# Kernel tuning notes

Measured on AMD Instinct MI355X. Metric: run time of the kernel, lower is better.

Reference implementation:

```python
import jax, jax.numpy as jnp
import numpy as np

B, Q, L = 256, 32, 40      # batch, num concept queries, text seq len
VW, TW, D = 768, 768, 256  # vision width, text width, contrastive embed dim


def setup_inputs() -> dict:
    key = jax.random.key(0)
    ks = jax.random.split(key, 5)
    concept_feat = jax.random.normal(ks[0], (B, Q, VW), jnp.float32)
    text_embeds = jax.random.normal(ks[1], (B, L, TW), jnp.float32)
    # contiguous attention masks: [CLS] tok ... [SEP] pad pad
    lengths = jax.random.randint(ks[2], (B,), 8, L + 1)
    text_mask = (jnp.arange(L)[None, :] < lengths[:, None]).astype(jnp.int32)
    Wc = jax.random.normal(ks[3], (VW, D), jnp.float32) * 0.02
    bc = jnp.zeros((D,), jnp.float32)
    Ww = jax.random.normal(ks[4], (TW, D), jnp.float32) * 0.02
    bw = jnp.zeros((D,), jnp.float32)
    temp_cpt = jnp.float32(0.07)
    return {"concept_feat": concept_feat, "text_embeds": text_embeds,
            "text_mask": text_mask, "Wc": Wc, "bc": bc, "Ww": Ww, "bw": bw,
            "temp_cpt": temp_cpt}


def _l2norm(x):
    return x / jnp.linalg.norm(x, axis=-1, keepdims=True)


def _remove_cls_sep(mask):
    # zero [CLS] (pos 0) and [SEP] (last nonzero position)
    m = mask.at[:, 0].set(0)
    Ls = m.shape[1]
    sep = (Ls - 1) - jnp.argmax(m[:, ::-1] > 0, axis=1)  # max nonzero index
    return m * (1 - jax.nn.one_hot(sep, Ls, dtype=m.dtype))


def _pair_sim(ref, ref_mask, cand, cand_mask):
    # ref: [Br,Sr,D] plays the 'visual_output' role, cand: [Bc,Sc,D] the
    # 'sequence_output' role of max_region_sum_word, vectorized over Br.
    A = jnp.einsum('bsd,ctd->bcst', ref, cand)  # [Br,Bc,Sr,Sc]
    valid = (ref_mask[:, None, :, None] > 0) & (cand_mask[None, :, None, :] > 0)
    A = jnp.where(valid, A, jnp.asarray(-2.0, A.dtype))
    row = A.max(axis=2)                          # [Br,Bc,Sc] max over ref pos
    n_words = (row > -2).sum(-1).astype(A.dtype)
    row = jnp.where(row < -1, 0.0, row).sum(-1) / n_words
    col = A.max(axis=3)                          # [Br,Bc,Sr] max over cand pos
    n_ref = (col > -2).sum(-1).astype(A.dtype)
    col = jnp.where(col < -1, 0.0, col).sum(-1) / n_ref
    return row + col                             # [Br,Bc]


def reference(concept_feat, text_embeds, text_mask, Wc, bc, Ww, bw, temp_cpt):
    cf = _l2norm(concept_feat @ Wc + bc)   # [B,Q,D]
    wf = _l2norm(text_embeds @ Ww + bw)    # [B,L,D]
    c_mask = jnp.ones(cf.shape[:-1], jnp.int32)
    w_mask = _remove_cls_sep(text_mask)
    # single device: AllGather is identity, rank 0
    sim_i2t = _pair_sim(cf, c_mask, wf, w_mask) / temp_cpt  # [B,B]
    sim_t2i = _pair_sim(wf, w_mask, cf, c_mask) / temp_cpt  # [B,B]
    # diagonal one-hot targets -> loss is -mean(diag(log_softmax))
    loss_i2t = -jnp.mean(jnp.diagonal(jax.nn.log_softmax(sim_i2t, axis=1)))
    loss_t2i = -jnp.mean(jnp.diagonal(jax.nn.log_softmax(sim_t2i, axis=1)))
    return (loss_i2t + loss_t2i) / 2
```

## Files before the change

kernel.cpp:

```cpp
#include <hip/hip_runtime.h>
#include <hip/hip_bf16.h>
#include <stdint.h>


using f32x4  = __attribute__((ext_vector_type(4))) float;
using bf16x8 = __attribute__((ext_vector_type(8))) short;
typedef unsigned uint32x2 __attribute__((ext_vector_type(2)));

__device__ __forceinline__ short f2bf(float f) {
  union { float f; uint32_t u; } x; x.f = f;
  uint32_t r = x.u + 0x7FFFu + ((x.u >> 16) & 1u);
  return (short)(r >> 16);
}

__device__ __forceinline__ bf16x8 pack8pk(float4 v0, float4 v1) {
  union { uint32_t u[4]; bf16x8 v; } r;
  asm("v_cvt_pk_bf16_f32 %0, %1, %2" : "=v"(r.u[0]) : "v"(v0.x), "v"(v0.y));
  asm("v_cvt_pk_bf16_f32 %0, %1, %2" : "=v"(r.u[1]) : "v"(v0.z), "v"(v0.w));
  asm("v_cvt_pk_bf16_f32 %0, %1, %2" : "=v"(r.u[2]) : "v"(v1.x), "v"(v1.y));
  asm("v_cvt_pk_bf16_f32 %0, %1, %2" : "=v"(r.u[3]) : "v"(v1.z), "v"(v1.w));
  return r.v;
}

__device__ __forceinline__ void gl_lds16(const unsigned short* g, unsigned short* l) {
  __builtin_amdgcn_global_load_lds(
      (const __attribute__((address_space(1))) void*)g,
      (__attribute__((address_space(3))) void*)l, 16, 0, 0);
}

template <int CTRL>
__device__ __forceinline__ float dppf(float x) {
  return __int_as_float(__builtin_amdgcn_update_dpp(
      0, __float_as_int(x), CTRL, 0xF, 0xF, true));
}
__device__ __forceinline__ float max16(float x) {
  x = fmaxf(x, dppf<0xB1>(x));
  x = fmaxf(x, dppf<0x4E>(x));
  x = fmaxf(x, dppf<0x141>(x));
  x = fmaxf(x, dppf<0x140>(x));
  return x;
}
__device__ __forceinline__ float sum16(float x) {
  x += dppf<0xB1>(x);
  x += dppf<0x4E>(x);
  x += dppf<0x141>(x);
  x += dppf<0x140>(x);
  return x;
}
__device__ __forceinline__ float rowsum_to63(float x) {
  x += dppf<0x142>(x);
  x += dppf<0x143>(x);
  return x;
}

#if __has_builtin(__builtin_amdgcn_permlane16_swap)
__device__ __forceinline__ float plmax16(float x) {
  uint32x2 r = __builtin_amdgcn_permlane16_swap(__float_as_uint(x), __float_as_uint(x), false, false);
  return fmaxf(__uint_as_float(r[0]), __uint_as_float(r[1]));
}
#else
__device__ __forceinline__ float plmax16(float x) { return fmaxf(x, __shfl_xor(x, 16)); }
#endif
#if __has_builtin(__builtin_amdgcn_permlane32_swap)
__device__ __forceinline__ float plmax32(float x) {
  uint32x2 r = __builtin_amdgcn_permlane32_swap(__float_as_uint(x), __float_as_uint(x), false, false);
  return fmaxf(__uint_as_float(r[0]), __uint_as_float(r[1]));
}
#else
__device__ __forceinline__ float plmax32(float x) { return fmaxf(x, __shfl_xor(x, 32)); }
#endif

__global__ __launch_bounds__(256) void k_trw(const float* __restrict__ Wc,
                                             const float* __restrict__ Ww,
                                             const int* __restrict__ tm,
                                             unsigned short* __restrict__ Wct,
                                             unsigned short* __restrict__ Wwt,
                                             unsigned long long* __restrict__ mb,
                                             float* __restrict__ nw) {
  __shared__ float tile[32][33];
  if (blockIdx.x == 0) {
    int b = threadIdx.x;
    unsigned long long bits = 0ull;
    int sep = -1;
    #pragma unroll
    for (int t = 1; t < 40; ++t) {
      if (tm[b * 40 + t] > 0) { bits |= (1ull << t); sep = t; }
    }
    if (sep >= 0) bits &= ~(1ull << sep);
    mb[b] = bits;
    nw[b] = 1.0f / (float)__popcll(bits);
  }
  int blk = blockIdx.x;
  const float* W; unsigned short* O;
  if (blk < 192) { W = Wc; O = Wct; } else { W = Ww; O = Wwt; blk -= 192; }
  const int tk = blk >> 3, td = blk & 7;
  const int k0 = tk * 32, d0 = td * 32;
  const int t = threadIdx.x;
  const int r = t >> 3, cq = (t & 7) * 4;
  float4 v = *(const float4*)(W + (size_t)(k0 + r) * 256 + d0 + cq);
  tile[r][cq] = v.x; tile[r][cq + 1] = v.y; tile[r][cq + 2] = v.z; tile[r][cq + 3] = v.w;
  __syncthreads();
  ushort4 o;
  o.x = (unsigned short)f2bf(tile[cq + 0][r]);
  o.y = (unsigned short)f2bf(tile[cq + 1][r]);
  o.z = (unsigned short)f2bf(tile[cq + 2][r]);
  o.w = (unsigned short)f2bf(tile[cq + 3][r]);
  *(ushort4*)(O + (size_t)(d0 + r) * 768 + k0 + cq) = o;
}

__global__ __launch_bounds__(256) void k_proj(const float* __restrict__ Xc,
                                              const float* __restrict__ Xt,
                                              const unsigned short* __restrict__ Wct,
                                              const unsigned short* __restrict__ Wwt,
                                              const float* __restrict__ bc,
                                              const float* __restrict__ bw,
                                              unsigned short* __restrict__ CFb,
                                              unsigned short* __restrict__ WFb) {
  __shared__ unsigned short As[32 * 768];
  __shared__ float red[32][4];
  const int blk = blockIdx.x;
  const float* X; const unsigned short* Wtb; const float* bias;
  unsigned short* out; int m0;
  if (blk < 256) { X = Xc; Wtb = Wct; bias = bc; out = CFb; m0 = blk * 32; }
  else           { X = Xt; Wtb = Wwt; bias = bw; out = WFb; m0 = (blk - 256) * 32; }

  const int t = threadIdx.x;
  #pragma unroll
  for (int i = 0; i < 12; ++i) {
    int ch = i * 256 + t;
    int r = ch / 96, c = ch - r * 96;
    const float* p = X + (size_t)(m0 + r) * 768 + c * 8;
    bf16x8 v = pack8pk(*(const float4*)p, *(const float4*)(p + 4));
    *(bf16x8*)(&As[r * 768 + ((c ^ (r & 7)) * 8)]) = v;
  }
  __syncthreads();

  const int w = t >> 6, l = t & 63;
  const int lr = l & 15, lg = l >> 4;
  const int n0 = w * 64;

  f32x4 acc[2][4];
  #pragma unroll
  for (int mi = 0; mi < 2; ++mi)
    #pragma unroll
    for (int ni = 0; ni < 4; ++ni) acc[mi][ni] = f32x4{0.f, 0.f, 0.f, 0.f};

  const int r0 = lr, r1 = 16 + lr;

  #pragma unroll 4
  for (int ks = 0; ks < 24; ++ks) {
    const int c16 = ks * 4 + lg;
    bf16x8 a0 = *(const bf16x8*)(&As[r0 * 768 + ((c16 ^ (r0 & 7)) * 8)]);
    bf16x8 a1 = *(const bf16x8*)(&As[r1 * 768 + ((c16 ^ (r1 & 7)) * 8)]);
    bf16x8 bb[4];
    #pragma unroll
    for (int ni = 0; ni < 4; ++ni)
      bb[ni] = *(const bf16x8*)(Wtb + (size_t)(n0 + ni * 16 + lr) * 768 + ks * 32 + lg * 8);
    #pragma unroll
    for (int ni = 0; ni < 4; ++ni)
      acc[0][ni] = __builtin_amdgcn_mfma_f32_16x16x32_bf16(a0, bb[ni], acc[0][ni], 0, 0, 0);
    #pragma unroll
    for (int ni = 0; ni < 4; ++ni)
      acc[1][ni] = __builtin_amdgcn_mfma_f32_16x16x32_bf16(a1, bb[ni], acc[1][ni], 0, 0, 0);
  }

  float bv[4];
  #pragma unroll
  for (int ni = 0; ni < 4; ++ni) bv[ni] = bias[n0 + ni * 16 + lr];

  float ss[2][4];
  #pragma unroll
  for (int mi = 0; mi < 2; ++mi)
    #pragma unroll
    for (int j = 0; j < 4; ++j) {
      float s = 0.f;
      #pragma unroll
      for (int ni = 0; ni < 4; ++ni) {
        acc[mi][ni][j] += bv[ni];
        s += acc[mi][ni][j] * acc[mi][ni][j];
      }
      ss[mi][j] = s;
    }
  #pragma unroll
  for (int m = 1; m <= 8; m <<= 1)
    #pragma unroll
    for (int mi = 0; mi < 2; ++mi)
      #pragma unroll
      for (int j = 0; j < 4; ++j)
        ss[mi][j] += __shfl_xor(ss[mi][j], m);
  if (lr == 0) {
    #pragma unroll
    for (int mi = 0; mi < 2; ++mi)
      #pragma unroll
      for (int j = 0; j < 4; ++j)
        red[mi * 16 + lg * 4 + j][w] = ss[mi][j];
  }
  __syncthreads();
  #pragma unroll
  for (int mi = 0; mi < 2; ++mi)
    #pragma unroll
    for (int j = 0; j < 4; ++j) {
      int r = mi * 16 + lg * 4 + j;
      float sc = rsqrtf(red[r][0] + red[r][1] + red[r][2] + red[r][3]);
      #pragma unroll
      for (int ni = 0; ni < 4; ++ni)
        out[(size_t)(m0 + r) * 256 + n0 + ni * 16 + lr] =
            (unsigned short)f2bf(acc[mi][ni][j] * sc);
    }
}

__global__ __launch_bounds__(512, 2) void k_pair(const unsigned short* __restrict__ CF,
                                                 const unsigned short* __restrict__ WF,
                                                 const unsigned long long* __restrict__ MB,
                                                 const float* __restrict__ NW,
                                                 const float* __restrict__ TEMP,
                                                 float* __restrict__ S,
                                                 float* __restrict__ St) {
  __shared__ unsigned short wfs[40960];
  const int tid = threadIdx.x;
  const int w = tid >> 6, l = tid & 63;
  const int lr = l & 15, lg = l >> 4;
  const int b0 = blockIdx.x * 16, c0 = blockIdx.y * 16;
  const float invt = 1.0f / TEMP[0];
  const float s32 = invt * 0.03125f;

  const int sti = w >> 1, sth = w & 1;
  {
    const int cq = c0;
    #pragma unroll
    for (int j = 0; j < 10; ++j) {
      int t = sth * 20 + j * 2 + (l >> 5), sl = l & 31;
      gl_lds16(WF + ((size_t)(cq + sti) * 40 + t) * 256 + ((sl ^ (t & 7)) * 8),
               &wfs[sti * 10240 + sth * 5120 + j * 512]);
    }
  }

  bf16x8 a[2][2][8];
  #pragma unroll
  for (int bi = 0; bi < 2; ++bi) {
    const int b = b0 + w * 2 + bi;
    #pragma unroll
    for (int mi = 0; mi < 2; ++mi)
      #pragma unroll
      for (int ks = 0; ks < 8; ++ks)
        a[bi][mi][ks] = *(const bf16x8*)(CF + (size_t)(b * 32 + mi * 16 + lr) * 256 + (ks * 4 + lg) * 8);
  }

  int lbase[3][2];
  #pragma unroll
  for (int ni = 0; ni < 3; ++ni) {
    int t = ni * 16 + lr; if (t > 39) t = 39;
    int x = t & 7;
    #pragma unroll
    for (int p = 0; p < 2; ++p)
      lbase[ni][p] = t * 512 + ((lg ^ (x & 3)) * 16) + ((p ^ ((x >> 2) & 1)) * 64);
  }
  const char* ldsb = (const char*)wfs;

  asm volatile("s_waitcnt vmcnt(0)" ::: "memory");
  __syncthreads();

  #pragma unroll 1
  for (int pn = 0; pn < 4; ++pn) {
    const int cq = c0 + pn * 4;
    if (pn > 0) {
      __syncthreads();
      #pragma unroll
      for (int j = 0; j < 10; ++j) {
        int t = sth * 20 + j * 2 + (l >> 5), sl = l & 31;
        gl_lds16(WF + ((size_t)(cq + sti) * 40 + t) * 256 + ((sl ^ (t & 7)) * 8),
                 &wfs[sti * 10240 + sth * 5120 + j * 512]);
      }
      asm volatile("s_waitcnt vmcnt(0)" ::: "memory");
      __syncthreads();
    }

    #pragma unroll
    for (int ci = 0; ci < 4; ++ci) {
      const int cg = cq + ci;

      f32x4 acc[2][2][3];
      #pragma unroll
      for (int bi = 0; bi < 2; ++bi)
        #pragma unroll
        for (int mi = 0; mi < 2; ++mi)
          #pragma unroll
          for (int ni = 0; ni < 3; ++ni) acc[bi][mi][ni] = f32x4{0.f, 0.f, 0.f, 0.f};

      __builtin_amdgcn_s_setprio(1);
      #pragma unroll
      for (int ks = 0; ks < 8; ++ks) {
        const int p = ks & 1, k = ks >> 1;
        bf16x8 bfv[3];
        #pragma unroll
        for (int ni = 0; ni < 3; ++ni)
          bfv[ni] = *(const bf16x8*)(ldsb + lbase[ni][p] + k * 128 + ci * 20480);
        #pragma unroll
        for (int bi = 0; bi < 2; ++bi)
          #pragma unroll
          for (int mi = 0; mi < 2; ++mi)
            #pragma unroll
            for (int ni = 0; ni < 3; ++ni)
              acc[bi][mi][ni] = __builtin_amdgcn_mfma_f32_16x16x32_bf16(a[bi][mi][ks], bfv[ni], acc[bi][mi][ni], 0, 0, 0);
      }
      __builtin_amdgcn_s_setprio(0);

      const unsigned long long vb = MB[cg];
      const float inw = invt * NW[cg];
      bool val[3];
      #pragma unroll
      for (int ni = 0; ni < 3; ++ni) {
        int t = ni * 16 + lr;
        val[ni] = (t < 40) && ((vb >> t) & 1ull);
      }

      #pragma unroll
      for (int bi = 0; bi < 2; ++bi) {
        const int b = b0 + w * 2 + bi;

        float rp[2][4];
        #pragma unroll
        for (int mi = 0; mi < 2; ++mi)
          #pragma unroll
          for (int j = 0; j < 4; ++j) {
            float v0 = val[0] ? acc[bi][mi][0][j] : -2.0f;
            float v1 = val[1] ? acc[bi][mi][1][j] : -2.0f;
            float v2 = val[2] ? acc[bi][mi][2][j] : -2.0f;
            rp[mi][j] = max16(fmaxf(fmaxf(v0, v1), v2));
          }
        float rsum = rp[0][0] + rp[0][1] + rp[0][2] + rp[0][3]
                   + rp[1][0] + rp[1][1] + rp[1][2] + rp[1][3];
        rsum = rowsum_to63(rsum);

        float cp[3];
        #pragma unroll
        for (int ni = 0; ni < 3; ++ni) {
          float m = fmaxf(fmaxf(fmaxf(acc[bi][0][ni][0], acc[bi][0][ni][1]),
                                fmaxf(acc[bi][0][ni][2], acc[bi][0][ni][3])),
                          fmaxf(fmaxf(acc[bi][1][ni][0], acc[bi][1][ni][1]),
                                fmaxf(acc[bi][1][ni][2], acc[bi][1][ni][3])));
          m = plmax16(m);
          m = plmax32(m);
          cp[ni] = val[ni] ? m : 0.0f;
        }
        float csum = sum16(cp[0] + cp[1] + cp[2]);

        float sv = rsum * s32 + csum * inw;
        if (l == 63) {
          S [(size_t)b  * 256 + cg] = sv;
          St[(size_t)cg * 256 + b ] = sv;
        }
      }
    }
  }
}

__global__ __launch_bounds__(256) void k_loss1(const float* __restrict__ S,
                                               const float* __restrict__ St,
                                               float* __restrict__ v) {
  __shared__ float lred[2][4], sred[2][4];
  const int b = blockIdx.x, j = threadIdx.x;
  const int w = j >> 6, l = j & 63;
  float s1v = S [(size_t)b * 256 + j];
  float s2v = St[(size_t)b * 256 + j];
  float m1 = s1v, m2 = s2v;
  #pragma unroll
  for (int m = 1; m < 64; m <<= 1) {
    m1 = fmaxf(m1, __shfl_xor(m1, m));
    m2 = fmaxf(m2, __shfl_xor(m2, m));
  }
  if (l == 0) { lred[0][w] = m1; lred[1][w] = m2; }
  __syncthreads();
  m1 = fmaxf(fmaxf(lred[0][0], lred[0][1]), fmaxf(lred[0][2], lred[0][3]));
  m2 = fmaxf(fmaxf(lred[1][0], lred[1][1]), fmaxf(lred[1][2], lred[1][3]));
  float e1 = expf(s1v - m1), e2 = expf(s2v - m2);
  #pragma unroll
  for (int m = 1; m < 64; m <<= 1) {
    e1 += __shfl_xor(e1, m);
    e2 += __shfl_xor(e2, m);
  }
  if (l == 0) { sred[0][w] = e1; sred[1][w] = e2; }
  __syncthreads();
  if (j == 0) {
    float s1 = sred[0][0] + sred[0][1] + sred[0][2] + sred[0][3];
    float s2 = sred[1][0] + sred[1][1] + sred[1][2] + sred[1][3];
    v[b] = (m1 + logf(s1)) + (m2 + logf(s2)) - 2.0f * S[(size_t)b * 257];
  }
}

__global__ __launch_bounds__(256) void k_loss2(const float* __restrict__ v,
                                               float* __restrict__ out) {
  __shared__ float r[4];
  const int j = threadIdx.x;
  float x = v[j];
  #pragma unroll
  for (int m = 1; m < 64; m <<= 1) x += __shfl_xor(x, m);
  if ((j & 63) == 0) r[j >> 6] = x;
  __syncthreads();
  if (j == 0) out[0] = (r[0] + r[1] + r[2] + r[3]) * (1.0f / 512.0f);
}

extern "C" void kernel_launch(void* const* d_in, const int* in_sizes, int n_in,
                              void* d_out, int out_size, void* d_ws, size_t ws_size,
                              hipStream_t stream) {
  const float* concept = (const float*)d_in[0];
  const float* text    = (const float*)d_in[1];
  const int*   tmask   = (const int*)d_in[2];
  const float* Wc      = (const float*)d_in[3];
  const float* bc      = (const float*)d_in[4];
  const float* Ww      = (const float*)d_in[5];
  const float* bw      = (const float*)d_in[6];
  const float* temp    = (const float*)d_in[7];
  float* out = (float*)d_out;
  char* ws = (char*)d_ws;

  float*              Sm   = (float*)(ws + 0);
  float*              Stm  = (float*)(ws + 262144);
  unsigned short*     Wctb = (unsigned short*)(ws + 524288);
  unsigned short*     Wwtb = (unsigned short*)(ws + 917504);
  unsigned short*     CFb  = (unsigned short*)(ws + 1310720);
  unsigned short*     WFb  = (unsigned short*)(ws + 5505024);
  unsigned long long* MBp  = (unsigned long long*)(ws + 10747904);
  float*              NWp  = (float*)(ws + 10749952);
  float*              Vb   = (float*)(ws + 10751104);

  k_trw<<<384, 256, 0, stream>>>(Wc, Ww, tmask, Wctb, Wwtb, MBp, NWp);
  k_proj<<<576, 256, 0, stream>>>(concept, text, Wctb, Wwtb, bc, bw, CFb, WFb);
  dim3 pg(16, 16);
  k_pair<<<pg, 512, 0, stream>>>(CFb, WFb, MBp, NWp, temp, Sm, Stm);
  k_loss1<<<256, 256, 0, stream>>>(Sm, Stm, Vb);
  k_loss2<<<1, 256, 0, stream>>>(Vb, out);
}
```

Before: 117.7 us.

## Double the pair-kernel grid and software-pipeline reductions behind MFMAs

The pair kernel grid goes from 16x16 to 16x32 blocks, so each block handles 8 candidate texts instead of 16 and runs two LDS reload phases instead of four. The cross-lane max/sum reductions for text c are deferred and done after the MFMAs for text c+1, with partial maxima held in registers. The second tile's global-to-LDS load is issued before the last deferred reduction so the two overlap. The setprio hints are removed. The costs are more registers per thread and A-fragment loads repeated across twice as many blocks.

After: 138.2 us. 17.4% more time.

```diff
diff --git a/kernel.cpp b/kernel.cpp
--- a/kernel.cpp
+++ b/kernel.cpp
@@ -220,19 +220,16 @@
   const int tid = threadIdx.x;
   const int w = tid >> 6, l = tid & 63;
   const int lr = l & 15, lg = l >> 4;
-  const int b0 = blockIdx.x * 16, c0 = blockIdx.y * 16;
+  const int b0 = blockIdx.x * 16, c0 = blockIdx.y * 8;
   const float invt = 1.0f / TEMP[0];
   const float s32 = invt * 0.03125f;
 
   const int sti = w >> 1, sth = w & 1;
-  {
-    const int cq = c0;
-    #pragma unroll
-    for (int j = 0; j < 10; ++j) {
-      int t = sth * 20 + j * 2 + (l >> 5), sl = l & 31;
-      gl_lds16(WF + ((size_t)(cq + sti) * 40 + t) * 256 + ((sl ^ (t & 7)) * 8),
-               &wfs[sti * 10240 + sth * 5120 + j * 512]);
-    }
+  #pragma unroll
+  for (int j = 0; j < 10; ++j) {
+    int t = sth * 20 + j * 2 + (l >> 5), sl = l & 31;
+    gl_lds16(WF + ((size_t)(c0 + sti) * 40 + t) * 256 + ((sl ^ (t & 7)) * 8),
+             &wfs[sti * 10240 + sth * 5120 + j * 512]);
   }
 
   bf16x8 a[2][2][8];
@@ -257,23 +254,15 @@
   }
   const char* ldsb = (const char*)wfs;
 
+  float Prp[2][2][2][4];
+  float Pcm[2][2][3];
+
   asm volatile("s_waitcnt vmcnt(0)" ::: "memory");
   __syncthreads();
 
   #pragma unroll 1
-  for (int pn = 0; pn < 4; ++pn) {
+  for (int pn = 0; pn < 2; ++pn) {
     const int cq = c0 + pn * 4;
-    if (pn > 0) {
-      __syncthreads();
-      #pragma unroll
-      for (int j = 0; j < 10; ++j) {
-        int t = sth * 20 + j * 2 + (l >> 5), sl = l & 31;
-        gl_lds16(WF + ((size_t)(cq + sti) * 40 + t) * 256 + ((sl ^ (t & 7)) * 8),
-                 &wfs[sti * 10240 + sth * 5120 + j * 512]);
-      }
-      asm volatile("s_waitcnt vmcnt(0)" ::: "memory");
-      __syncthreads();
-    }
 
     #pragma unroll
     for (int ci = 0; ci < 4; ++ci) {
@@ -287,7 +276,6 @@
           #pragma unroll
           for (int ni = 0; ni < 3; ++ni) acc[bi][mi][ni] = f32x4{0.f, 0.f, 0.f, 0.f};
 
-      __builtin_amdgcn_s_setprio(1);
       #pragma unroll
       for (int ks = 0; ks < 8; ++ks) {
         const int p = ks & 1, k = ks >> 1;
@@ -303,54 +291,120 @@
             for (int ni = 0; ni < 3; ++ni)
               acc[bi][mi][ni] = __builtin_amdgcn_mfma_f32_16x16x32_bf16(a[bi][mi][ks], bfv[ni], acc[bi][mi][ni], 0, 0, 0);
       }
-      __builtin_amdgcn_s_setprio(0);
-
-      const unsigned long long vb = MB[cg];
-      const float inw = invt * NW[cg];
-      bool val[3];
+
+      if (ci > 0) {
+        const int pg = cg - 1;
+        const int pb = (ci + 1) & 1;
+        const unsigned long long vbP = MB[pg];
+        const float inwP = invt * NW[pg];
+        bool valP[3];
+        #pragma unroll
+        for (int ni = 0; ni < 3; ++ni) {
+          int t = ni * 16 + lr;
+          valP[ni] = (t < 40) && ((vbP >> t) & 1ull);
+        }
+        #pragma unroll
+        for (int bi = 0; bi < 2; ++bi) {
+          const int b = b0 + w * 2 + bi;
+          float rsum = 0.f;
+          #pragma unroll
+          for (int mi = 0; mi < 2; ++mi)
+            #pragma unroll
+            for (int j = 0; j < 4; ++j)
+              rsum += max16(Prp[pb][bi][mi][j]);
+          rsum = rowsum_to63(rsum);
+          float cp[3];
+          #pragma unroll
+          for (int ni = 0; ni < 3; ++ni) {
+            float m = plmax32(plmax16(Pcm[pb][bi][ni]));
+            cp[ni] = valP[ni] ? m : 0.0f;
+          }
+          float csum = sum16(cp[0] + cp[1] + cp[2]);
+          float sv = rsum * s32 + csum * inwP;
+          if (l == 63) {
+            S [(size_t)b  * 256 + pg] = sv;
+            St[(size_t)pg * 256 + b ] = sv;
+          }
+        }
+      }
+
+      {
+        const int cb = ci & 1;
+        const unsigned long long vbC = MB[cg];
+        bool valC[3];
+        #pragma unroll
+        for (int ni = 0; ni < 3; ++ni) {
+          int t = ni * 16 + lr;
+          valC[ni] = (t < 40) && ((vbC >> t) & 1ull);
+        }
+        #pragma unroll
+        for (int bi = 0; bi < 2; ++bi) {
+          #pragma unroll
+          for (int mi = 0; mi < 2; ++mi)
+            #pragma unroll
+            for (int j = 0; j < 4; ++j) {
+              float v0 = valC[0] ? acc[bi][mi][0][j] : -2.0f;
+              float v1 = valC[1] ? acc[bi][mi][1][j] : -2.0f;
+              float v2 = valC[2] ? acc[bi][mi][2][j] : -2.0f;
+              Prp[cb][bi][mi][j] = fmaxf(fmaxf(v0, v1), v2);
+            }
+          #pragma unroll
+          for (int ni = 0; ni < 3; ++ni)
+            Pcm[cb][bi][ni] =
+                fmaxf(fmaxf(fmaxf(acc[bi][0][ni][0], acc[bi][0][ni][1]),
+                            fmaxf(acc[bi][0][ni][2], acc[bi][0][ni][3])),
+                      fmaxf(fmaxf(acc[bi][1][ni][0], acc[bi][1][ni][1]),
+                            fmaxf(acc[bi][1][ni][2], acc[bi][1][ni][3])));
+        }
+      }
+    }
+
+    if (pn == 0) {
+      __syncthreads();
+      #pragma unroll
+      for (int j = 0; j < 10; ++j) {
+        int t = sth * 20 + j * 2 + (l >> 5), sl = l & 31;
+        gl_lds16(WF + ((size_t)(cq + 4 + sti) * 40 + t) * 256 + ((sl ^ (t & 7)) * 8),
+                 &wfs[sti * 10240 + sth * 5120 + j * 512]);
+      }
+    }
+    {
+      const int pg = cq + 3;
+      const unsigned long long vbP = MB[pg];
+      const float inwP = invt * NW[pg];
+      bool valP[3];
       #pragma unroll
       for (int ni = 0; ni < 3; ++ni) {
         int t = ni * 16 + lr;
-        val[ni] = (t < 40) && ((vb >> t) & 1ull);
-      }
-
+        valP[ni] = (t < 40) && ((vbP >> t) & 1ull);
+      }
       #pragma unroll
       for (int bi = 0; bi < 2; ++bi) {
         const int b = b0 + w * 2 + bi;
-
-        float rp[2][4];
+        float rsum = 0.f;
         #pragma unroll
         for (int mi = 0; mi < 2; ++mi)
           #pragma unroll
-          for (int j = 0; j < 4; ++j) {
-            float v0 = val[0] ? acc[bi][mi][0][j] : -2.0f;
-            float v1 = val[1] ? acc[bi][mi][1][j] : -2.0f;
-            float v2 = val[2] ? acc[bi][mi][2][j] : -2.0f;
-            rp[mi][j] = max16(fmaxf(fmaxf(v0, v1), v2));
-          }
-        float rsum = rp[0][0] + rp[0][1] + rp[0][2] + rp[0][3]
-                   + rp[1][0] + rp[1][1] + rp[1][2] + rp[1][3];
+          for (int j = 0; j < 4; ++j)
+            rsum += max16(Prp[1][bi][mi][j]);
         rsum = rowsum_to63(rsum);
-
         float cp[3];
         #pragma unroll
         for (int ni = 0; ni < 3; ++ni) {
-          float m = fmaxf(fmaxf(fmaxf(acc[bi][0][ni][0], acc[bi][0][ni][1]),
-                                fmaxf(acc[bi][0][ni][2], acc[bi][0][ni][3])),
-                          fmaxf(fmaxf(acc[bi][1][ni][0], acc[bi][1][ni][1]),
-                                fmaxf(acc[bi][1][ni][2], acc[bi][1][ni][3])));
-          m = plmax16(m);
-          m = plmax32(m);
-          cp[ni] = val[ni] ? m : 0.0f;
+          float m = plmax32(plmax16(Pcm[1][bi][ni]));
+          cp[ni] = valP[ni] ? m : 0.0f;
         }
         float csum = sum16(cp[0] + cp[1] + cp[2]);
-
-        float sv = rsum * s32 + csum * inw;
+        float sv = rsum * s32 + csum * inwP;
         if (l == 63) {
-          S [(size_t)b  * 256 + cg] = sv;
-          St[(size_t)cg * 256 + b ] = sv;
-        }
-      }
+          S [(size_t)b  * 256 + pg] = sv;
+          St[(size_t)pg * 256 + b ] = sv;
+        }
+      }
+    }
+    if (pn == 0) {
+      asm volatile("s_waitcnt vmcnt(0)" ::: "memory");
+      __syncthreads();
     }
   }
 }
@@ -426,7 +480,7 @@
 
   k_trw<<<384, 256, 0, stream>>>(Wc, Ww, tmask, Wctb, Wwtb, MBp, NWp);
   k_proj<<<576, 256, 0, stream>>>(concept, text, Wctb, Wwtb, bc, bw, CFb, WFb);
-  dim3 pg(16, 16);
+  dim3 pg(16, 32);
   k_pair<<<pg, 512, 0, stream>>>(CFb, WFb, MBp, NWp, temp, Sm, Stm);
   k_loss1<<<256, 256, 0, stream>>>(Sm, Stm, Vb);
   k_loss2<<<1, 256, 0, stream>>>(Vb, out);
```
